# Optimization experiments

Measured on AMD Instinct MI355X. Metric: run time of the kernel, lower is better.

## Reference

```python
import jax, jax.numpy as jnp
import numpy as np

S, D_MODEL, D_RNN = 256, 512, 512  # module's broadcasting requires d_rnn == d_model


def setup_inputs() -> dict:
    key = jax.random.key(0)
    k1, k2, k3, k4 = jax.random.split(key, 4)
    x = jax.random.normal(k1, (S, D_MODEL), dtype=jnp.float32)
    state = jnp.zeros((D_RNN, D_MODEL), dtype=jnp.float32)
    # equinox nn.Linear default init: U[-1/sqrt(in), 1/sqrt(in)] for weight and bias
    lim = 1.0 / np.sqrt(D_MODEL)
    W1 = jax.random.uniform(k2, (2 * D_RNN, D_MODEL), minval=-lim, maxval=lim, dtype=jnp.float32)
    b1 = jax.random.uniform(k3, (2 * D_RNN,), minval=-lim, maxval=lim, dtype=jnp.float32)
    # Lambda init exactly as in source: inv_sigmoid(p) = log(1/(1-p)), bounds ** (1/8)
    inv_sig = lambda p: np.log(1.0 / (1.0 - p))
    lower = float(np.power(inv_sig(0.9), 1.0 / 8.0))
    upper = float(np.power(inv_sig(0.999), 1.0 / 8.0))
    Lambda = jax.random.uniform(k4, (D_MODEL,), minval=lower, maxval=upper, dtype=jnp.float32)
    return {"x": x, "state": state, "W1": W1, "b1": b1, "Lambda": Lambda}


def reference(x, state, W1, b1, Lambda):
    # lin1 applied per timestep: (S, d_model) @ (d_model, 2*d_rnn)
    z = jax.nn.sigmoid(x @ W1.T + b1)              # (S, 2*d_rnn)
    inp, rec = jnp.split(z, 2, axis=-1)            # each (S, d_rnn)
    # recurrence gate a_t in (0,1): exp(-8 * softplus(Lambda) * rec)
    a = jnp.exp(-8.0 * jax.nn.softplus(Lambda)[None, :] * rec)  # (S, d_rnn)
    # gated input: outer product per step -> (S, d_rnn, d_model)
    gated_x = jnp.einsum('is,is,id->isd', jnp.sqrt(1.0 - a * a), inp, x)

    def step(h, xs):
        g, at = xs
        h = at[:, None] * h + g                    # (d_rnn, d_model)
        return h, h

    state, y = jax.lax.scan(step, state, (gated_x, a))
    return (y, state)
```

## Files before the change

kernel.cpp:

```cpp
#include <hip/hip_runtime.h>
#include <hip/hip_bf16.h>

#define S_LEN 256
#define DM    512
#define DR    512


__global__ __launch_bounds__(256) void k_transpose_x(const float* __restrict__ x,
                                                     float* __restrict__ xT) {
    __shared__ float tile[32][33];
    const int k0 = blockIdx.x * 32;
    const int t0 = blockIdx.y * 32;
    const int lx = threadIdx.x & 31;
    const int ly = threadIdx.x >> 5;
#pragma unroll
    for (int i = 0; i < 32; i += 8)
        tile[ly + i][lx] = x[(t0 + ly + i) * DM + k0 + lx];
    __syncthreads();
#pragma unroll
    for (int i = 0; i < 32; i += 8)
        xT[(k0 + ly + i) * S_LEN + t0 + lx] = tile[lx][ly + i];
}

__global__ __launch_bounds__(256) void k_gemm(const float* __restrict__ xT,
                                              const float* __restrict__ W1,
                                              float* __restrict__ part) {
    const int ng = blockIdx.x;
    const int ks = blockIdx.y;
    const int t  = threadIdx.x;
    const int k0 = ks * 256;

    float acc[8] = {0.f, 0.f, 0.f, 0.f, 0.f, 0.f, 0.f, 0.f};
    const float* __restrict__ wb = W1 + (ng * 8) * DM + k0;
    const float* __restrict__ xb = xT + k0 * S_LEN + t;

#pragma unroll 8
    for (int k = 0; k < 256; ++k) {
        const float xv = xb[k * S_LEN];
#pragma unroll
        for (int j = 0; j < 8; ++j)
            acc[j] = fmaf(xv, wb[j * DM + k], acc[j]);
    }

    float* __restrict__ pb = part + ks * (1024 * 256) + (ng * 8) * 256 + t;
#pragma unroll
    for (int j = 0; j < 8; ++j) pb[j * 256] = acc[j];
}

__global__ __launch_bounds__(256) void k_act(const float* __restrict__ part,
                                             const float* __restrict__ b1,
                                             const float* __restrict__ Lam,
                                             float* __restrict__ aT,
                                             float* __restrict__ cT) {
    const int s = blockIdx.x;
    const int t = threadIdx.x;
    const int P2 = 1024 * 256;

    const float pre_i = part[s * 256 + t] + part[P2 + s * 256 + t] + b1[s];
    const float pre_r = part[(512 + s) * 256 + t] + part[P2 + (512 + s) * 256 + t] + b1[512 + s];

    const float inp = 1.f / (1.f + expf(-pre_i));
    const float rec = 1.f / (1.f + expf(-pre_r));
    const float sp  = log1pf(expf(Lam[s]));
    const float a   = expf(-8.f * sp * rec);
    const float c   = sqrtf(fmaxf(1.f - a * a, 0.f)) * inp;

    aT[s * 256 + t] = a;
    cT[s * 256 + t] = c;
}

__global__ __launch_bounds__(256) void k_rec(const float* __restrict__ x,
                                             const float* __restrict__ state0,
                                             const float* __restrict__ aT,
                                             const float* __restrict__ cT,
                                             float2* __restrict__ out2) {
    const int s   = blockIdx.x;
    const int tid = threadIdx.x;

    __shared__ float a_l[256];
    __shared__ float c_l[256];
    a_l[tid] = aT[s * 256 + tid];
    c_l[tid] = cT[s * 256 + tid];
    __syncthreads();

    const float2* __restrict__ st2 = reinterpret_cast<const float2*>(state0);
    float2 h = st2[s * 256 + tid];

    const float2* __restrict__ x2 = reinterpret_cast<const float2*>(x);

#pragma unroll 8
    for (int t = 0; t < S_LEN; ++t) {
        const float at = a_l[t];
        const float ct = c_l[t];
        const float2 xv = x2[t * 256 + tid];
        h.x = fmaf(at, h.x, ct * xv.x);
        h.y = fmaf(at, h.y, ct * xv.y);
        out2[t * (DR * DM / 2) + s * 256 + tid] = h;
    }
    out2[(S_LEN * DR * DM / 2) + s * 256 + tid] = h;
}

extern "C" void kernel_launch(void* const* d_in, const int* in_sizes, int n_in,
                              void* d_out, int out_size, void* d_ws, size_t ws_size,
                              hipStream_t stream) {
    const float* x      = (const float*)d_in[0];
    const float* state0 = (const float*)d_in[1];
    const float* W1     = (const float*)d_in[2];
    const float* b1     = (const float*)d_in[3];
    const float* Lam    = (const float*)d_in[4];

    float* ws   = (float*)d_ws;
    float* xT   = ws;
    float* part = ws + 131072;
    float* aT   = ws + 655360;
    float* cT   = ws + 786432;

    float2* out2 = (float2*)d_out;

    k_transpose_x<<<dim3(16, 8), 256, 0, stream>>>(x, xT);
    k_gemm<<<dim3(128, 2), 256, 0, stream>>>(xT, W1, part);
    k_act<<<dim3(512), 256, 0, stream>>>(part, b1, Lam, aT, cT);
    k_rec<<<dim3(512), 256, 0, stream>>>(x, state0, aT, cT, out2);
}
```

Measured before the change: 78.45 us.

## Fuse GEMM with activation, interleave gate arrays, vectorize recurrence stores

Merges the split-K GEMM and the activation kernel into one kernel, where each block computes the full K reduction for two channel pairs and applies the sigmoid/exp gating in registers. This removes the partial-sum round trip and one launch. The a and c gates are packed into a single float2 array. The recurrence kernel now handles two channels per block with float4 lanes, prefetches the next x row, and writes output with nontemporal stores to cut instruction count and cache pollution on the large output write. In exchange, the GEMM has less parallelism (256 blocks over the full K), and the recurrence launches half as many blocks.

```diff
diff --git a/kernel.cpp b/kernel.cpp
--- a/kernel.cpp
+++ b/kernel.cpp
@@ -4,6 +4,9 @@
 #define S_LEN 256
 #define DM    512
 #define DR    512
+
+typedef float f4 __attribute__((ext_vector_type(4)));
+typedef float f2 __attribute__((ext_vector_type(2)));
 
 
 __global__ __launch_bounds__(256) void k_transpose_x(const float* __restrict__ x,
@@ -22,82 +25,84 @@
         xT[(k0 + ly + i) * S_LEN + t0 + lx] = tile[lx][ly + i];
 }
 
-__global__ __launch_bounds__(256) void k_gemm(const float* __restrict__ xT,
-                                              const float* __restrict__ W1,
-                                              float* __restrict__ part) {
-    const int ng = blockIdx.x;
-    const int ks = blockIdx.y;
+__global__ __launch_bounds__(256) void k_gemm_act(const float* __restrict__ xT,
+                                                  const float* __restrict__ W1,
+                                                  const float* __restrict__ b1,
+                                                  const float* __restrict__ Lam,
+                                                  f2* __restrict__ acT) {
+    const int g  = blockIdx.x;
     const int t  = threadIdx.x;
-    const int k0 = ks * 256;
+    const int r0 = 2 * g;
 
-    float acc[8] = {0.f, 0.f, 0.f, 0.f, 0.f, 0.f, 0.f, 0.f};
-    const float* __restrict__ wb = W1 + (ng * 8) * DM + k0;
-    const float* __restrict__ xb = xT + k0 * S_LEN + t;
+    float acc0 = 0.f, acc1 = 0.f, acc2 = 0.f, acc3 = 0.f;
+    const float* __restrict__ xb = xT + t;
+    const float* __restrict__ w0 = W1 + (r0)       * DM;
+    const float* __restrict__ w1 = W1 + (r0 + 1)   * DM;
+    const float* __restrict__ w2 = W1 + (512 + r0) * DM;
+    const float* __restrict__ w3 = W1 + (513 + r0) * DM;
 
 #pragma unroll 8
-    for (int k = 0; k < 256; ++k) {
+    for (int k = 0; k < DM; ++k) {
         const float xv = xb[k * S_LEN];
-#pragma unroll
-        for (int j = 0; j < 8; ++j)
-            acc[j] = fmaf(xv, wb[j * DM + k], acc[j]);
+        acc0 = fmaf(xv, w0[k], acc0);
+        acc1 = fmaf(xv, w1[k], acc1);
+        acc2 = fmaf(xv, w2[k], acc2);
+        acc3 = fmaf(xv, w3[k], acc3);
     }
 
-    float* __restrict__ pb = part + ks * (1024 * 256) + (ng * 8) * 256 + t;
 #pragma unroll
-    for (int j = 0; j < 8; ++j) pb[j * 256] = acc[j];
-}
-
-__global__ __launch_bounds__(256) void k_act(const float* __restrict__ part,
-                                             const float* __restrict__ b1,
-                                             const float* __restrict__ Lam,
-                                             float* __restrict__ aT,
-                                             float* __restrict__ cT) {
-    const int s = blockIdx.x;
-    const int t = threadIdx.x;
-    const int P2 = 1024 * 256;
-
-    const float pre_i = part[s * 256 + t] + part[P2 + s * 256 + t] + b1[s];
-    const float pre_r = part[(512 + s) * 256 + t] + part[P2 + (512 + s) * 256 + t] + b1[512 + s];
-
-    const float inp = 1.f / (1.f + expf(-pre_i));
-    const float rec = 1.f / (1.f + expf(-pre_r));
-    const float sp  = log1pf(expf(Lam[s]));
-    const float a   = expf(-8.f * sp * rec);
-    const float c   = sqrtf(fmaxf(1.f - a * a, 0.f)) * inp;
-
-    aT[s * 256 + t] = a;
-    cT[s * 256 + t] = c;
+    for (int j = 0; j < 2; ++j) {
+        const float pre_i = (j ? acc1 : acc0) + b1[r0 + j];
+        const float pre_r = (j ? acc3 : acc2) + b1[512 + r0 + j];
+        const float inp = 1.f / (1.f + expf(-pre_i));
+        const float rec = 1.f / (1.f + expf(-pre_r));
+        const float sp  = log1pf(expf(Lam[r0 + j]));
+        const float a   = expf(-8.f * sp * rec);
+        const float c   = sqrtf(fmaxf(1.f - a * a, 0.f)) * inp;
+        f2 ac; ac.x = a; ac.y = c;
+        acT[(r0 + j) * S_LEN + t] = ac;
+    }
 }
 
 __global__ __launch_bounds__(256) void k_rec(const float* __restrict__ x,
                                              const float* __restrict__ state0,
-                                             const float* __restrict__ aT,
-                                             const float* __restrict__ cT,
-                                             float2* __restrict__ out2) {
-    const int s   = blockIdx.x;
-    const int tid = threadIdx.x;
+                                             const f2* __restrict__ acT,
+                                             f4* __restrict__ out4) {
+    const int bx   = blockIdx.x;
+    const int tid  = threadIdx.x;
+    const int half = tid >> 7;
+    const int s    = bx * 2 + half;
+    const int dq   = tid & 127;
 
-    __shared__ float a_l[256];
-    __shared__ float c_l[256];
-    a_l[tid] = aT[s * 256 + tid];
-    c_l[tid] = cT[s * 256 + tid];
+    __shared__ f2 ac_l[2][S_LEN];
+    f2* lf = &ac_l[0][0];
+    lf[tid]       = acT[bx * 2 * S_LEN + tid];
+    lf[tid + 256] = acT[bx * 2 * S_LEN + tid + 256];
     __syncthreads();
 
-    const float2* __restrict__ st2 = reinterpret_cast<const float2*>(state0);
-    float2 h = st2[s * 256 + tid];
+    const f4* __restrict__ st4 = reinterpret_cast<const f4*>(state0);
+    f4 h = st4[s * 128 + dq];
 
-    const float2* __restrict__ x2 = reinterpret_cast<const float2*>(x);
+    const f4* __restrict__ x4 = reinterpret_cast<const f4*>(x);
+    f4 xv = x4[dq];
 
-#pragma unroll 8
+#pragma unroll 4
     for (int t = 0; t < S_LEN; ++t) {
-        const float at = a_l[t];
-        const float ct = c_l[t];
-        const float2 xv = x2[t * 256 + tid];
+        f4 xn;
+        if (t + 1 < S_LEN) xn = x4[(t + 1) * 128 + dq];
+        else xn = (f4)0.f;
+
+        const f2 ac = ac_l[half][t];
+        const float at = ac.x, ct = ac.y;
         h.x = fmaf(at, h.x, ct * xv.x);
         h.y = fmaf(at, h.y, ct * xv.y);
-        out2[t * (DR * DM / 2) + s * 256 + tid] = h;
+        h.z = fmaf(at, h.z, ct * xv.z);
+        h.w = fmaf(at, h.w, ct * xv.w);
+
+        __builtin_nontemporal_store(h, &out4[(t * DR + s) * 128 + dq]);
+        xv = xn;
     }
-    out2[(S_LEN * DR * DM / 2) + s * 256 + tid] = h;
+    out4[(S_LEN * DR) * 128 + s * 128 + dq] = h;
 }
 
 extern "C" void kernel_launch(void* const* d_in, const int* in_sizes, int n_in,
@@ -109,16 +114,13 @@
     const float* b1     = (const float*)d_in[3];
     const float* Lam    = (const float*)d_in[4];
 
-    float* ws   = (float*)d_ws;
-    float* xT   = ws;
-    float* part = ws + 131072;
-    float* aT   = ws + 655360;
-    float* cT   = ws + 786432;
+    float* ws  = (float*)d_ws;
+    float* xT  = ws;
+    f2*    acT = (f2*)(ws + 131072);
 
-    float2* out2 = (float2*)d_out;
+    f4* out4 = (f4*)d_out;
 
     k_transpose_x<<<dim3(16, 8), 256, 0, stream>>>(x, xT);
-    k_gemm<<<dim3(128, 2), 256, 0, stream>>>(xT, W1, part);
-    k_act<<<dim3(512), 256, 0, stream>>>(part, b1, Lam, aT, cT);
-    k_rec<<<dim3(512), 256, 0, stream>>>(x, state0, aT, cT, out2);
+    k_gemm_act<<<dim3(256), 256, 0, stream>>>(xT, W1, b1, Lam, acT);
+    k_rec<<<dim3(256), 256, 0, stream>>>(x, state0, acT, out4);
 }
```

Result: faster. 74.48 us (-5.1%).
